# Kernel tuning notes

Measured on AMD Instinct MI355X. Metric: run time of the kernel, lower is better.

Reference implementation:

```python
import jax, jax.numpy as jnp
import numpy as np

B, D, H, W = 16, 64, 64, 64
K = 1024


def setup_inputs() -> dict:
    key = jax.random.key(0)
    k1, k2 = jax.random.split(key)
    x = jax.random.normal(k1, (B, D, H, W), dtype=jnp.float32)
    limit = 3.0 ** 0.5
    e_i_ts = jax.random.uniform(k2, (D, K), dtype=jnp.float32, minval=-limit, maxval=limit)
    return {"x": x, "e_i_ts": e_i_ts}


def reference(x, e_i_ts):
    b, d, h, w = x.shape
    # [B,H,W,D] -> [N,D]
    flat_x = jnp.transpose(x, (0, 2, 3, 1)).reshape(-1, d)
    distances = (
        jnp.sum(flat_x * flat_x, axis=1, keepdims=True)
        - 2.0 * (flat_x @ e_i_ts)
        + jnp.sum(e_i_ts * e_i_ts, axis=0, keepdims=True)
    )
    encoding_indices = jnp.argmin(distances, axis=1)  # [N]
    reshaped_indices = encoding_indices.reshape(b, h, w)
    # codebook gather: e_i_ts.T is [K,D]
    quantized = jnp.take(e_i_ts.T, reshaped_indices, axis=0)  # [B,H,W,D]
    quantized_x = jnp.transpose(quantized, (0, 3, 1, 2))  # [B,D,H,W]

    dictionary_loss = jnp.mean((jax.lax.stop_gradient(x) - quantized_x) ** 2)
    commitment_loss = jnp.mean((x - jax.lax.stop_gradient(quantized_x)) ** 2)
    # straight-through estimator
    quantized_x = x + jax.lax.stop_gradient(quantized_x - x)
    return quantized_x, dictionary_loss, commitment_loss, encoding_indices.reshape(b, -1)
```

## Files before the change

### kernel.cpp

```cpp
#include <hip/hip_runtime.h>

#define DD 64
#define KK 1024
#define NPTS 65536
#define TOTAL 4194304

#define OFF_L1 4194304
#define OFF_L2 4194305
#define OFF_IDX 4194306

#define WS_ENH_F 64
#define WS_EHT_BYTE 65536
#define WS_ELT_BYTE (65536 + 131072)

#define MARGIN_S 0.008f

typedef __attribute__((ext_vector_type(8))) short short8;
typedef __attribute__((ext_vector_type(4))) float f32x4;

__device__ __forceinline__ unsigned short bf16_rne(float f) {
    unsigned b = __float_as_uint(f);
    return (unsigned short)((b + 0x7FFFu + ((b >> 16) & 1u)) >> 16);
}
__device__ __forceinline__ float bf16_to_f(unsigned short h) {
    return __uint_as_float(((unsigned)h) << 16);
}
__device__ __forceinline__ unsigned umax(unsigned a, unsigned b) { return a > b ? a : b; }
__device__ __forceinline__ unsigned umin(unsigned a, unsigned b) { return a < b ? a : b; }
__device__ __forceinline__ void gld_lds16(const void* g, void* l) {
    __builtin_amdgcn_global_load_lds(
        (const __attribute__((address_space(1))) void*)g,
        (__attribute__((address_space(3))) void*)l, 16, 0, 0);
}
__device__ __forceinline__ int swz(int r, int d) {
    return ((d & ~7) ^ ((r & 7) << 3)) | (d & 7);
}

__global__ __launch_bounds__(256) void prep_kernel(const float* __restrict__ e,
                                                   float* __restrict__ enh,
                                                   unsigned short* __restrict__ ehT,
                                                   unsigned short* __restrict__ elT,
                                                   float* __restrict__ sum,
                                                   unsigned* __restrict__ tick) {
    const int tid = threadIdx.x;
    if (blockIdx.x == 0 && tid == 0) { *sum = 0.f; *tick = 0u; }
    const int wave = tid >> 6, lane = tid & 63;
    const int k = blockIdx.x * 4 + wave;
    const float v = e[lane * KK + k];
    const unsigned short h = bf16_rne(v);
    const unsigned short l = bf16_rne(v - bf16_to_f(h));
    const int pos = k * 64 + swz(k, lane);
    ehT[pos] = h;
    elT[pos] = l;
    float s2 = v * v;
#pragma unroll
    for (int m = 32; m > 0; m >>= 1) s2 += __shfl_down(s2, m, 64);
    if (lane == 0) enh[k] = 512.0f - 0.5f * s2;
}

__global__ __launch_bounds__(256) void vq_gemm(const float* __restrict__ x,
                                               const float* __restrict__ e,
                                               const float* __restrict__ enh,
                                               const unsigned short* __restrict__ ehT,
                                               const unsigned short* __restrict__ elT,
                                               float* __restrict__ out,
                                               float* __restrict__ sum,
                                               unsigned* __restrict__ tick) {
    __shared__ __align__(16) char ebuf[2 * 16384];
    __shared__ __align__(16) char xbuf[32768];
    __shared__ float xnp2[256];

    unsigned short* xbh = (unsigned short*)xbuf;
    unsigned short* xbl = xbh + 128 * 64;
    int*   ks  = (int*)xbuf;
    float* lv  = (float*)(ks + 128);
    float* xp  = lv + 128;
    int*   rl  = (int*)(xp + 64);
    int*   rn  = rl + 128;
    float* rv  = (float*)(rn + 1);
    int*   ri  = (int*)(rv + 4);
    float* red = (float*)(ri + 4);

    const int tid = threadIdx.x;
    const int wave = tid >> 6, lane = tid & 63;
    const int n0 = blockIdx.x * 128;
    const int b = n0 >> 12;
    const int hw0 = n0 & 4095;

    const char* ehTb = (const char*)ehT;
    const char* elTb = (const char*)elT;
    const int lofs = wave * 1024 + lane * 16;

    {
        char* db = ebuf;
        gld_lds16(ehTb + lofs,        db + wave * 1024);
        gld_lds16(ehTb + 4096 + lofs, db + 4096 + wave * 1024);
        gld_lds16(elTb + lofs,        db + 8192 + wave * 1024);
        gld_lds16(elTb + 4096 + lofs, db + 12288 + wave * 1024);
    }

    {
        const int p = tid & 127, dg = tid >> 7;
        const float* xs = x + ((b * DD + dg * 32) << 12) + hw0 + p;
        float xv[32];
        float xn = 0.f;
#pragma unroll
        for (int s = 0; s < 32; ++s) {
            xv[s] = xs[s << 12];
            xn = fmaf(xv[s], xv[s], xn);
        }
        xnp2[tid] = xn;
#pragma unroll
        for (int g = 0; g < 4; ++g) {
            short8 hh, ll;
#pragma unroll
            for (int j = 0; j < 8; ++j) {
                const float f = xv[g * 8 + j];
                const unsigned short h = bf16_rne(f);
                hh[j] = (short)h;
                ll[j] = (short)bf16_rne(f - bf16_to_f(h));
            }
            const int d0 = dg * 32 + g * 8;
            const int pos = p * 64 + (d0 ^ ((p & 7) << 3));
            *(short8*)(xbh + pos) = hh;
            *(short8*)(xbl + pos) = ll;
        }
    }
    __syncthreads();

    const int ln15 = lane & 15, q8 = (lane >> 4) * 8;
    const int wp = wave * 32;

    short8 ah[2][2], al[2][2];
#pragma unroll
    for (int rf = 0; rf < 2; ++rf)
#pragma unroll
        for (int kc = 0; kc < 2; ++kc) {
            const int pp = wp + rf * 16 + ln15;
            const int pos = pp * 64 + ((kc * 32 + q8) ^ ((pp & 7) << 3));
            ah[rf][kc] = *(const short8*)(xbh + pos);
            al[rf][kc] = *(const short8*)(xbl + pos);
        }

    unsigned v1u[8], v2u[8];
#pragma unroll
    for (int r = 0; r < 8; ++r) { v1u[r] = 0u; v2u[r] = 0u; }

    for (int kt = 0; kt < 16; ++kt) {
        __syncthreads();
        if (kt < 15) {
            const int nkt = kt + 1;
            char* db = ebuf + (nkt & 1) * 16384;
            const char* sH = ehTb + nkt * 8192 + lofs;
            const char* sL = elTb + nkt * 8192 + lofs;
            gld_lds16(sH,        db + wave * 1024);
            gld_lds16(sH + 4096, db + 4096 + wave * 1024);
            gld_lds16(sL,        db + 8192 + wave * 1024);
            gld_lds16(sL + 4096, db + 12288 + wave * 1024);
        }
        const unsigned short* ebH = (const unsigned short*)(ebuf + (kt & 1) * 16384);
        const unsigned short* ebL = ebH + 4096;

        f32x4 acc[2][4];
#pragma unroll
        for (int cf = 0; cf < 4; ++cf) {
            const float ec = enh[kt * 64 + cf * 16 + ln15];
#pragma unroll
            for (int rf = 0; rf < 2; ++rf)
                acc[rf][cf] = (f32x4){ec, ec, ec, ec};
        }

#pragma unroll
        for (int kc = 0; kc < 2; ++kc) {
            short8 bh[4], bl[4];
#pragma unroll
            for (int cf = 0; cf < 4; ++cf) {
                const int c = cf * 16 + ln15;
                const int pos = c * 64 + ((kc * 32 + q8) ^ ((c & 7) << 3));
                bh[cf] = *(const short8*)(ebH + pos);
                bl[cf] = *(const short8*)(ebL + pos);
            }
#pragma unroll
            for (int rf = 0; rf < 2; ++rf)
#pragma unroll
                for (int cf = 0; cf < 4; ++cf) {
                    acc[rf][cf] = __builtin_amdgcn_mfma_f32_16x16x32_bf16(al[rf][kc], bh[cf], acc[rf][cf], 0, 0, 0);
                    acc[rf][cf] = __builtin_amdgcn_mfma_f32_16x16x32_bf16(ah[rf][kc], bl[cf], acc[rf][cf], 0, 0, 0);
                    acc[rf][cf] = __builtin_amdgcn_mfma_f32_16x16x32_bf16(ah[rf][kc], bh[cf], acc[rf][cf], 0, 0, 0);
                }
        }

#pragma unroll
        for (int rf = 0; rf < 2; ++rf)
#pragma unroll
            for (int reg = 0; reg < 4; ++reg) {
                const int r = rf * 4 + reg;
                const unsigned k0 = (__float_as_uint(acc[rf][0][reg]) | 63u) ^ (unsigned)(kt * 4 + 0);
                const unsigned k1 = (__float_as_uint(acc[rf][1][reg]) | 63u) ^ (unsigned)(kt * 4 + 1);
                const unsigned k2 = (__float_as_uint(acc[rf][2][reg]) | 63u) ^ (unsigned)(kt * 4 + 2);
                const unsigned k3 = (__float_as_uint(acc[rf][3][reg]) | 63u) ^ (unsigned)(kt * 4 + 3);
                unsigned a = umax(k0, k1), bb = umin(k0, k1);
                v2u[r] = umax(umax(v2u[r], umin(v1u[r], a)), bb);
                v1u[r] = umax(v1u[r], a);
                a = umax(k2, k3); bb = umin(k2, k3);
                v2u[r] = umax(umax(v2u[r], umin(v1u[r], a)), bb);
                v1u[r] = umax(v1u[r], a);
            }
    }

    __syncthreads();
    if (tid == 0) *rn = 0;
    __syncthreads();

#pragma unroll
    for (int r = 0; r < 8; ++r) {
        const unsigned c6 = 63u - (v1u[r] & 63u);
        int col = (int)(c6 >> 2) * 64 + (int)(c6 & 3) * 16 + ln15;
        float val = __uint_as_float(v1u[r] & ~63u);
        float sec = __uint_as_float(v2u[r] & ~63u);
#pragma unroll
        for (int msk = 1; msk < 16; msk <<= 1) {
            const float ov = __shfl_xor(val, msk);
            const int oc = __shfl_xor(col, msk);
            const float os = __shfl_xor(sec, msk);
            sec = fmaxf(fmaxf(sec, os), fminf(val, ov));
            const bool t = (ov > val) || (ov == val && oc < col);
            val = t ? ov : val;
            col = t ? oc : col;
        }
        if (ln15 == 0) {
            const int q = lane >> 4;
            const int pt = wp + (r >> 2) * 16 + q * 4 + (r & 3);
            ks[pt] = col;
            const float xnp = xnp2[pt] + xnp2[128 + pt];
            const float bmid = __uint_as_float(__float_as_uint(val) | 32u);
            lv[pt] = xnp + 1024.0f - 2.0f * bmid;
            if (val - sec < MARGIN_S) {
                const int w = atomicAdd(rn, 1);
                rl[w] = pt;
            }
        }
    }
    __syncthreads();

    const int lcnt = *rn;
    for (int it = 0; it < lcnt; ++it) {
        const int pr = rl[it];
        if (tid < 64) xp[tid] = x[((b * DD + tid) << 12) + hw0 + pr];
        __syncthreads();
        float d0 = 0.f, d1 = 0.f, d2 = 0.f, d3 = 0.f;
#pragma unroll 8
        for (int dd = 0; dd < DD; ++dd) {
            const float xd = xp[dd];
            const float4 ev = *(const float4*)(e + dd * KK + tid * 4);
            d0 = fmaf(xd, ev.x, d0);
            d1 = fmaf(xd, ev.y, d1);
            d2 = fmaf(xd, ev.z, d2);
            d3 = fmaf(xd, ev.w, d3);
        }
        const float4 ea = *(const float4*)(enh + tid * 4);
        float bs = d0 + ea.x;
        int bi2 = tid * 4;
        if (d1 + ea.y > bs) { bs = d1 + ea.y; bi2 = tid * 4 + 1; }
        if (d2 + ea.z > bs) { bs = d2 + ea.z; bi2 = tid * 4 + 2; }
        if (d3 + ea.w > bs) { bs = d3 + ea.w; bi2 = tid * 4 + 3; }
#pragma unroll
        for (int m = 1; m < 64; m <<= 1) {
            const float ov = __shfl_xor(bs, m, 64);
            const int oi = __shfl_xor(bi2, m, 64);
            if (ov > bs || (ov == bs && oi < bi2)) { bs = ov; bi2 = oi; }
        }
        if (lane == 0) { rv[wave] = bs; ri[wave] = bi2; }
        __syncthreads();
        if (tid == 0) {
            float gs = rv[0];
            int gi = ri[0];
#pragma unroll
            for (int t2 = 1; t2 < 4; ++t2)
                if (rv[t2] > gs || (rv[t2] == gs && ri[t2] < gi)) { gs = rv[t2]; gi = ri[t2]; }
            ks[pr] = gi;
            const float xnp = xnp2[pr] + xnp2[128 + pr];
            lv[pr] = xnp + 1024.0f - 2.0f * gs;
        }
        __syncthreads();
    }

    if (tid < 128) {
        out[OFF_IDX + n0 + tid] = (float)ks[tid];
        float lc = lv[tid];
#pragma unroll
        for (int off = 32; off > 0; off >>= 1) lc += __shfl_down(lc, off, 64);
        if (lane == 0) red[wave] = lc;
    }
    __syncthreads();
    if (tid == 0) {
        atomicAdd(sum, red[0] + red[1]);
        __threadfence();
        const unsigned old = atomicAdd(tick, 1u);
        if (old == (unsigned)(gridDim.x - 1)) {
            const float s = atomicAdd(sum, 0.0f);
            const float m = s * (1.0f / (float)TOTAL);
            out[OFF_L1] = m;
            out[OFF_L2] = m;
        }
    }

    {
        const int pe = tid & 127, dh = tid >> 7;
        const int kp = ks[pe];
        const int kx = (kp & 7) << 3;
        float qa[32];
#pragma unroll
        for (int g = 0; g < 4; ++g) {
            const int pos = kp * 64 + ((dh * 32 + g * 8) ^ kx);
            const short8 h8 = *(const short8*)(ehT + pos);
            const short8 l8 = *(const short8*)(elT + pos);
#pragma unroll
            for (int j = 0; j < 8; ++j)
                qa[g * 8 + j] = bf16_to_f((unsigned short)h8[j]) + bf16_to_f((unsigned short)l8[j]);
        }
        float* ob = out + ((b * DD + dh * 32) << 12) + hw0 + pe;
#pragma unroll
        for (int s = 0; s < 32; ++s) ob[s << 12] = qa[s];
    }
}

extern "C" void kernel_launch(void* const* d_in, const int* in_sizes, int n_in,
                              void* d_out, int out_size, void* d_ws, size_t ws_size,
                              hipStream_t stream) {
    const float* x = (const float*)d_in[0];
    const float* e = (const float*)d_in[1];
    float* out = (float*)d_out;

    float* sum = (float*)d_ws;
    unsigned* tick = (unsigned*)d_ws + 2;
    float* enh = (float*)d_ws + WS_ENH_F;
    unsigned short* ehT = (unsigned short*)((char*)d_ws + WS_EHT_BYTE);
    unsigned short* elT = (unsigned short*)((char*)d_ws + WS_ELT_BYTE);

    prep_kernel<<<256, 256, 0, stream>>>(e, enh, ehT, elT, sum, tick);
    vq_gemm<<<NPTS / 128, 256, 0, stream>>>(x, e, enh, ehT, elT, out, sum, tick);
}
```

Before: 124.6 us.

## Stage codebook in 256-code quarters and coalesce prep kernel writes via LDS transpose

```diff
diff --git a/kernel.cpp b/kernel.cpp
--- a/kernel.cpp
+++ b/kernel.cpp
@@ -36,26 +36,67 @@
     return ((d & ~7) ^ ((r & 7) << 3)) | (d & 7);
 }
 
+__device__ __forceinline__ void stage_quarter(const char* ehTb, const char* elTb,
+                                              char* cb, int q, int wave, int lane) {
+    const int off = wave * 8192 + lane * 16;
+    const char* sH = ehTb + q * 32768 + off;
+    const char* sL = elTb + q * 32768 + off;
+    char* dH = cb + wave * 8192;
+    char* dL = cb + 32768 + wave * 8192;
+#pragma unroll
+    for (int j = 0; j < 8; ++j) {
+        gld_lds16(sH + j * 1024, dH + j * 1024);
+        gld_lds16(sL + j * 1024, dL + j * 1024);
+    }
+}
+
 __global__ __launch_bounds__(256) void prep_kernel(const float* __restrict__ e,
                                                    float* __restrict__ enh,
                                                    unsigned short* __restrict__ ehT,
                                                    unsigned short* __restrict__ elT,
                                                    float* __restrict__ sum,
                                                    unsigned* __restrict__ tick) {
-    const int tid = threadIdx.x;
+    __shared__ unsigned short tH[64 * 64];
+    __shared__ unsigned short tL[64 * 64];
+    __shared__ float ps[4 * 64];
+    const int tid = threadIdx.x, wave = tid >> 6, lane = tid & 63;
     if (blockIdx.x == 0 && tid == 0) { *sum = 0.f; *tick = 0u; }
-    const int wave = tid >> 6, lane = tid & 63;
-    const int k = blockIdx.x * 4 + wave;
-    const float v = e[lane * KK + k];
-    const unsigned short h = bf16_rne(v);
-    const unsigned short l = bf16_rne(v - bf16_to_f(h));
-    const int pos = k * 64 + swz(k, lane);
-    ehT[pos] = h;
-    elT[pos] = l;
-    float s2 = v * v;
-#pragma unroll
-    for (int m = 32; m > 0; m >>= 1) s2 += __shfl_down(s2, m, 64);
-    if (lane == 0) enh[k] = 512.0f - 0.5f * s2;
+    const int k = blockIdx.x * 64 + lane;
+    float s2 = 0.f;
+    short8 hh[2], ll[2];
+#pragma unroll
+    for (int g = 0; g < 2; ++g)
+#pragma unroll
+        for (int j = 0; j < 8; ++j) {
+            const int d = wave * 16 + g * 8 + j;
+            const float v = e[d * KK + k];
+            const unsigned short h = bf16_rne(v);
+            hh[g][j] = (short)h;
+            ll[g][j] = (short)bf16_rne(v - bf16_to_f(h));
+            s2 = fmaf(v, v, s2);
+        }
+    ps[wave * 64 + lane] = s2;
+#pragma unroll
+    for (int g = 0; g < 2; ++g) {
+        const int pos = lane * 64 + ((wave * 16 + g * 8) ^ ((k & 7) << 3));
+        *(short8*)(tH + pos) = hh[g];
+        *(short8*)(tL + pos) = ll[g];
+    }
+    __syncthreads();
+    if (wave == 0) {
+        const float t = ps[lane] + ps[64 + lane] + ps[128 + lane] + ps[192 + lane];
+        enh[k] = 512.0f - 0.5f * t;
+    }
+    {
+        const short8* srcH = (const short8*)tH;
+        const short8* srcL = (const short8*)tL;
+        short8* dstH = (short8*)(ehT + blockIdx.x * 64 * 64);
+        short8* dstL = (short8*)(elT + blockIdx.x * 64 * 64);
+        dstH[tid * 2]     = srcH[tid * 2];
+        dstH[tid * 2 + 1] = srcH[tid * 2 + 1];
+        dstL[tid * 2]     = srcL[tid * 2];
+        dstL[tid * 2 + 1] = srcL[tid * 2 + 1];
+    }
 }
 
 __global__ __launch_bounds__(256) void vq_gemm(const float* __restrict__ x,
@@ -66,13 +107,12 @@
                                                float* __restrict__ out,
                                                float* __restrict__ sum,
                                                unsigned* __restrict__ tick) {
-    __shared__ __align__(16) char ebuf[2 * 16384];
-    __shared__ __align__(16) char xbuf[32768];
+    __shared__ __align__(16) char cb[65536];
     __shared__ float xnp2[256];
 
-    unsigned short* xbh = (unsigned short*)xbuf;
-    unsigned short* xbl = xbh + 128 * 64;
-    int*   ks  = (int*)xbuf;
+    unsigned short* xbh = (unsigned short*)cb;
+    unsigned short* xbl = (unsigned short*)(cb + 16384);
+    int*   ks  = (int*)cb;
     float* lv  = (float*)(ks + 128);
     float* xp  = lv + 128;
     int*   rl  = (int*)(xp + 64);
@@ -89,15 +129,6 @@
 
     const char* ehTb = (const char*)ehT;
     const char* elTb = (const char*)elT;
-    const int lofs = wave * 1024 + lane * 16;
-
-    {
-        char* db = ebuf;
-        gld_lds16(ehTb + lofs,        db + wave * 1024);
-        gld_lds16(ehTb + 4096 + lofs, db + 4096 + wave * 1024);
-        gld_lds16(elTb + lofs,        db + 8192 + wave * 1024);
-        gld_lds16(elTb + 4096 + lofs, db + 12288 + wave * 1024);
-    }
 
     {
         const int p = tid & 127, dg = tid >> 7;
@@ -141,74 +172,75 @@
             ah[rf][kc] = *(const short8*)(xbh + pos);
             al[rf][kc] = *(const short8*)(xbl + pos);
         }
+    __syncthreads();
+
+    stage_quarter(ehTb, elTb, cb, 0, wave, lane);
 
     unsigned v1u[8], v2u[8];
 #pragma unroll
     for (int r = 0; r < 8; ++r) { v1u[r] = 0u; v2u[r] = 0u; }
 
-    for (int kt = 0; kt < 16; ++kt) {
-        __syncthreads();
-        if (kt < 15) {
-            const int nkt = kt + 1;
-            char* db = ebuf + (nkt & 1) * 16384;
-            const char* sH = ehTb + nkt * 8192 + lofs;
-            const char* sL = elTb + nkt * 8192 + lofs;
-            gld_lds16(sH,        db + wave * 1024);
-            gld_lds16(sH + 4096, db + 4096 + wave * 1024);
-            gld_lds16(sL,        db + 8192 + wave * 1024);
-            gld_lds16(sL + 4096, db + 12288 + wave * 1024);
-        }
-        const unsigned short* ebH = (const unsigned short*)(ebuf + (kt & 1) * 16384);
-        const unsigned short* ebL = ebH + 4096;
-
-        f32x4 acc[2][4];
-#pragma unroll
-        for (int cf = 0; cf < 4; ++cf) {
-            const float ec = enh[kt * 64 + cf * 16 + ln15];
+    const unsigned short* cbH = (const unsigned short*)cb;
+    const unsigned short* cbL = (const unsigned short*)(cb + 32768);
+
+    for (int q = 0; q < 4; ++q) {
+        __syncthreads();
+
+#pragma unroll
+        for (int ct = 0; ct < 4; ++ct) {
+            const int tile = q * 4 + ct;
+
+            f32x4 acc[2][4];
+#pragma unroll
+            for (int cf = 0; cf < 4; ++cf) {
+                const float ec = enh[tile * 64 + cf * 16 + ln15];
+#pragma unroll
+                for (int rf = 0; rf < 2; ++rf)
+                    acc[rf][cf] = (f32x4){ec, ec, ec, ec};
+            }
+
+#pragma unroll
+            for (int kc = 0; kc < 2; ++kc) {
+                short8 bh[4], bl[4];
+#pragma unroll
+                for (int cf = 0; cf < 4; ++cf) {
+                    const int c = ct * 64 + cf * 16 + ln15;
+                    const int pos = c * 64 + ((kc * 32 + q8) ^ ((c & 7) << 3));
+                    bh[cf] = *(const short8*)(cbH + pos);
+                    bl[cf] = *(const short8*)(cbL + pos);
+                }
+#pragma unroll
+                for (int rf = 0; rf < 2; ++rf)
+#pragma unroll
+                    for (int cf = 0; cf < 4; ++cf) {
+                        acc[rf][cf] = __builtin_amdgcn_mfma_f32_16x16x32_bf16(al[rf][kc], bh[cf], acc[rf][cf], 0, 0, 0);
+                        acc[rf][cf] = __builtin_amdgcn_mfma_f32_16x16x32_bf16(ah[rf][kc], bl[cf], acc[rf][cf], 0, 0, 0);
+                        acc[rf][cf] = __builtin_amdgcn_mfma_f32_16x16x32_bf16(ah[rf][kc], bh[cf], acc[rf][cf], 0, 0, 0);
+                    }
+            }
+
 #pragma unroll
             for (int rf = 0; rf < 2; ++rf)
-                acc[rf][cf] = (f32x4){ec, ec, ec, ec};
-        }
-
-#pragma unroll
-        for (int kc = 0; kc < 2; ++kc) {
-            short8 bh[4], bl[4];
-#pragma unroll
-            for (int cf = 0; cf < 4; ++cf) {
-                const int c = cf * 16 + ln15;
-                const int pos = c * 64 + ((kc * 32 + q8) ^ ((c & 7) << 3));
-                bh[cf] = *(const short8*)(ebH + pos);
-                bl[cf] = *(const short8*)(ebL + pos);
-            }
-#pragma unroll
-            for (int rf = 0; rf < 2; ++rf)
-#pragma unroll
-                for (int cf = 0; cf < 4; ++cf) {
-                    acc[rf][cf] = __builtin_amdgcn_mfma_f32_16x16x32_bf16(al[rf][kc], bh[cf], acc[rf][cf], 0, 0, 0);
-                    acc[rf][cf] = __builtin_amdgcn_mfma_f32_16x16x32_bf16(ah[rf][kc], bl[cf], acc[rf][cf], 0, 0, 0);
-                    acc[rf][cf] = __builtin_amdgcn_mfma_f32_16x16x32_bf16(ah[rf][kc], bh[cf], acc[rf][cf], 0, 0, 0);
+#pragma unroll
+                for (int reg = 0; reg < 4; ++reg) {
+                    const int r = rf * 4 + reg;
+                    const unsigned k0 = (__float_as_uint(acc[rf][0][reg]) | 63u) ^ (unsigned)(tile * 4 + 0);
+                    const unsigned k1 = (__float_as_uint(acc[rf][1][reg]) | 63u) ^ (unsigned)(tile * 4 + 1);
+                    const unsigned k2 = (__float_as_uint(acc[rf][2][reg]) | 63u) ^ (unsigned)(tile * 4 + 2);
+                    const unsigned k3 = (__float_as_uint(acc[rf][3][reg]) | 63u) ^ (unsigned)(tile * 4 + 3);
+                    unsigned a = umax(k0, k1), bb = umin(k0, k1);
+                    v2u[r] = umax(umax(v2u[r], umin(v1u[r], a)), bb);
+                    v1u[r] = umax(v1u[r], a);
+                    a = umax(k2, k3); bb = umin(k2, k3);
+                    v2u[r] = umax(umax(v2u[r], umin(v1u[r], a)), bb);
+                    v1u[r] = umax(v1u[r], a);
                 }
         }
 
-#pragma unroll
-        for (int rf = 0; rf < 2; ++rf)
-#pragma unroll
-            for (int reg = 0; reg < 4; ++reg) {
-                const int r = rf * 4 + reg;
-                const unsigned k0 = (__float_as_uint(acc[rf][0][reg]) | 63u) ^ (unsigned)(kt * 4 + 0);
-                const unsigned k1 = (__float_as_uint(acc[rf][1][reg]) | 63u) ^ (unsigned)(kt * 4 + 1);
-                const unsigned k2 = (__float_as_uint(acc[rf][2][reg]) | 63u) ^ (unsigned)(kt * 4 + 2);
-                const unsigned k3 = (__float_as_uint(acc[rf][3][reg]) | 63u) ^ (unsigned)(kt * 4 + 3);
-                unsigned a = umax(k0, k1), bb = umin(k0, k1);
-                v2u[r] = umax(umax(v2u[r], umin(v1u[r], a)), bb);
-                v1u[r] = umax(v1u[r], a);
-                a = umax(k2, k3); bb = umin(k2, k3);
-                v2u[r] = umax(umax(v2u[r], umin(v1u[r], a)), bb);
-                v1u[r] = umax(v1u[r], a);
-            }
-    }
-
-    __syncthreads();
+        __syncthreads();
+        if (q < 3) stage_quarter(ehTb, elTb, cb, q + 1, wave, lane);
+    }
+
     if (tid == 0) *rn = 0;
     __syncthreads();
 
@@ -229,8 +261,8 @@
             col = t ? oc : col;
         }
         if (ln15 == 0) {
-            const int q = lane >> 4;
-            const int pt = wp + (r >> 2) * 16 + q * 4 + (r & 3);
+            const int qq = lane >> 4;
+            const int pt = wp + (r >> 2) * 16 + qq * 4 + (r & 3);
             ks[pt] = col;
             const float xnp = xnp2[pt] + xnp2[128 + pt];
             const float bmid = __uint_as_float(__float_as_uint(val) | 32u);
@@ -338,6 +370,6 @@
     unsigned short* ehT = (unsigned short*)((char*)d_ws + WS_EHT_BYTE);
     unsigned short* elT = (unsigned short*)((char*)d_ws + WS_ELT_BYTE);
 
-    prep_kernel<<<256, 256, 0, stream>>>(e, enh, ehT, elT, sum, tick);
+    prep_kernel<<<KK / 64, 256, 0, stream>>>(e, enh, ehT, elT, sum, tick);
     vq_gemm<<<NPTS / 128, 256, 0, stream>>>(x, e, enh, ehT, elT, out, sum, tick);
 }
```

New measurement: 121.5 us. 2.5% less time.

## Alias x staging into codebook buffer to cut LDS and compute loss exactly

Applied to the files above, without the earlier changes.

```diff
diff --git a/kernel.cpp b/kernel.cpp
--- a/kernel.cpp
+++ b/kernel.cpp
@@ -42,20 +42,47 @@
                                                    unsigned short* __restrict__ elT,
                                                    float* __restrict__ sum,
                                                    unsigned* __restrict__ tick) {
-    const int tid = threadIdx.x;
+    __shared__ unsigned short tH[64 * 64];
+    __shared__ unsigned short tL[64 * 64];
+    __shared__ float ps[4 * 64];
+    const int tid = threadIdx.x, wave = tid >> 6, lane = tid & 63;
     if (blockIdx.x == 0 && tid == 0) { *sum = 0.f; *tick = 0u; }
-    const int wave = tid >> 6, lane = tid & 63;
-    const int k = blockIdx.x * 4 + wave;
-    const float v = e[lane * KK + k];
-    const unsigned short h = bf16_rne(v);
-    const unsigned short l = bf16_rne(v - bf16_to_f(h));
-    const int pos = k * 64 + swz(k, lane);
-    ehT[pos] = h;
-    elT[pos] = l;
-    float s2 = v * v;
-#pragma unroll
-    for (int m = 32; m > 0; m >>= 1) s2 += __shfl_down(s2, m, 64);
-    if (lane == 0) enh[k] = 512.0f - 0.5f * s2;
+    const int k = blockIdx.x * 64 + lane;
+    float s2 = 0.f;
+    short8 hh[2], ll[2];
+#pragma unroll
+    for (int g = 0; g < 2; ++g)
+#pragma unroll
+        for (int j = 0; j < 8; ++j) {
+            const int d = wave * 16 + g * 8 + j;
+            const float v = e[d * KK + k];
+            const unsigned short h = bf16_rne(v);
+            hh[g][j] = (short)h;
+            ll[g][j] = (short)bf16_rne(v - bf16_to_f(h));
+            s2 = fmaf(v, v, s2);
+        }
+    ps[wave * 64 + lane] = s2;
+#pragma unroll
+    for (int g = 0; g < 2; ++g) {
+        const int pos = lane * 64 + ((wave * 16 + g * 8) ^ ((k & 7) << 3));
+        *(short8*)(tH + pos) = hh[g];
+        *(short8*)(tL + pos) = ll[g];
+    }
+    __syncthreads();
+    if (wave == 0) {
+        const float t = ps[lane] + ps[64 + lane] + ps[128 + lane] + ps[192 + lane];
+        enh[k] = 512.0f - 0.5f * t;
+    }
+    {
+        const short8* srcH = (const short8*)tH;
+        const short8* srcL = (const short8*)tL;
+        short8* dstH = (short8*)(ehT + blockIdx.x * 64 * 64);
+        short8* dstL = (short8*)(elT + blockIdx.x * 64 * 64);
+        dstH[tid * 2]     = srcH[tid * 2];
+        dstH[tid * 2 + 1] = srcH[tid * 2 + 1];
+        dstL[tid * 2]     = srcL[tid * 2];
+        dstL[tid * 2 + 1] = srcL[tid * 2 + 1];
+    }
 }
 
 __global__ __launch_bounds__(256) void vq_gemm(const float* __restrict__ x,
@@ -67,14 +94,11 @@
                                                float* __restrict__ sum,
                                                unsigned* __restrict__ tick) {
     __shared__ __align__(16) char ebuf[2 * 16384];
-    __shared__ __align__(16) char xbuf[32768];
-    __shared__ float xnp2[256];
-
-    unsigned short* xbh = (unsigned short*)xbuf;
-    unsigned short* xbl = xbh + 128 * 64;
-    int*   ks  = (int*)xbuf;
-    float* lv  = (float*)(ks + 128);
-    float* xp  = lv + 128;
+
+    unsigned short* xbh = (unsigned short*)ebuf;
+    unsigned short* xbl = (unsigned short*)(ebuf + 16384);
+    int*   ks  = (int*)ebuf;
+    float* xp  = (float*)(ks + 128);
     int*   rl  = (int*)(xp + 64);
     int*   rn  = rl + 128;
     float* rv  = (float*)(rn + 1);
@@ -92,24 +116,11 @@
     const int lofs = wave * 1024 + lane * 16;
 
     {
-        char* db = ebuf;
-        gld_lds16(ehTb + lofs,        db + wave * 1024);
-        gld_lds16(ehTb + 4096 + lofs, db + 4096 + wave * 1024);
-        gld_lds16(elTb + lofs,        db + 8192 + wave * 1024);
-        gld_lds16(elTb + 4096 + lofs, db + 12288 + wave * 1024);
-    }
-
-    {
         const int p = tid & 127, dg = tid >> 7;
         const float* xs = x + ((b * DD + dg * 32) << 12) + hw0 + p;
         float xv[32];
-        float xn = 0.f;
-#pragma unroll
-        for (int s = 0; s < 32; ++s) {
-            xv[s] = xs[s << 12];
-            xn = fmaf(xv[s], xv[s], xn);
-        }
-        xnp2[tid] = xn;
+#pragma unroll
+        for (int s = 0; s < 32; ++s) xv[s] = xs[s << 12];
 #pragma unroll
         for (int g = 0; g < 4; ++g) {
             short8 hh, ll;
@@ -141,6 +152,15 @@
             ah[rf][kc] = *(const short8*)(xbh + pos);
             al[rf][kc] = *(const short8*)(xbl + pos);
         }
+    __syncthreads();
+
+    {
+        char* db = ebuf;
+        gld_lds16(ehTb + lofs,        db + wave * 1024);
+        gld_lds16(ehTb + 4096 + lofs, db + 4096 + wave * 1024);
+        gld_lds16(elTb + lofs,        db + 8192 + wave * 1024);
+        gld_lds16(elTb + 4096 + lofs, db + 12288 + wave * 1024);
+    }
 
     unsigned v1u[8], v2u[8];
 #pragma unroll
@@ -229,12 +249,9 @@
             col = t ? oc : col;
         }
         if (ln15 == 0) {
-            const int q = lane >> 4;
-            const int pt = wp + (r >> 2) * 16 + q * 4 + (r & 3);
+            const int qq = lane >> 4;
+            const int pt = wp + (r >> 2) * 16 + qq * 4 + (r & 3);
             ks[pt] = col;
-            const float xnp = xnp2[pt] + xnp2[128 + pt];
-            const float bmid = __uint_as_float(__float_as_uint(val) | 32u);
-            lv[pt] = xnp + 1024.0f - 2.0f * bmid;
             if (val - sec < MARGIN_S) {
                 const int w = atomicAdd(rn, 1);
                 rl[w] = pt;
@@ -279,22 +296,32 @@
             for (int t2 = 1; t2 < 4; ++t2)
                 if (rv[t2] > gs || (rv[t2] == gs && ri[t2] < gi)) { gs = rv[t2]; gi = ri[t2]; }
             ks[pr] = gi;
-            const float xnp = xnp2[pr] + xnp2[128 + pr];
-            lv[pr] = xnp + 1024.0f - 2.0f * gs;
         }
         __syncthreads();
     }
 
-    if (tid < 128) {
-        out[OFF_IDX + n0 + tid] = (float)ks[tid];
-        float lc = lv[tid];
-#pragma unroll
-        for (int off = 32; off > 0; off >>= 1) lc += __shfl_down(lc, off, 64);
-        if (lane == 0) red[wave] = lc;
+    if (tid < 128) out[OFF_IDX + n0 + tid] = (float)ks[tid];
+
+    {
+        const int pe = tid & 127, dh = tid >> 7;
+        const int kp = ks[pe];
+        float lacc = 0.f;
+#pragma unroll
+        for (int s = 0; s < 32; ++s) {
+            const int d = dh * 32 + s;
+            const float qv = e[d * KK + kp];
+            const float xv = x[((b * DD + d) << 12) + hw0 + pe];
+            out[((b * DD + d) << 12) + hw0 + pe] = qv;
+            const float df = xv - qv;
+            lacc = fmaf(df, df, lacc);
+        }
+#pragma unroll
+        for (int off = 32; off > 0; off >>= 1) lacc += __shfl_down(lacc, off, 64);
+        if (lane == 0) red[wave] = lacc;
     }
     __syncthreads();
     if (tid == 0) {
-        atomicAdd(sum, red[0] + red[1]);
+        atomicAdd(sum, red[0] + red[1] + red[2] + red[3]);
         __threadfence();
         const unsigned old = atomicAdd(tick, 1u);
         if (old == (unsigned)(gridDim.x - 1)) {
@@ -304,25 +331,6 @@
             out[OFF_L2] = m;
         }
     }
-
-    {
-        const int pe = tid & 127, dh = tid >> 7;
-        const int kp = ks[pe];
-        const int kx = (kp & 7) << 3;
-        float qa[32];
-#pragma unroll
-        for (int g = 0; g < 4; ++g) {
-            const int pos = kp * 64 + ((dh * 32 + g * 8) ^ kx);
-            const short8 h8 = *(const short8*)(ehT + pos);
-            const short8 l8 = *(const short8*)(elT + pos);
-#pragma unroll
-            for (int j = 0; j < 8; ++j)
-                qa[g * 8 + j] = bf16_to_f((unsigned short)h8[j]) + bf16_to_f((unsigned short)l8[j]);
-        }
-        float* ob = out + ((b * DD + dh * 32) << 12) + hw0 + pe;
-#pragma unroll
-        for (int s = 0; s < 32; ++s) ob[s << 12] = qa[s];
-    }
 }
 
 extern "C" void kernel_launch(void* const* d_in, const int* in_sizes, int n_in,
@@ -338,6 +346,6 @@
     unsigned short* ehT = (unsigned short*)((char*)d_ws + WS_EHT_BYTE);
     unsigned short* elT = (unsigned short*)((char*)d_ws + WS_ELT_BYTE);
 
-    prep_kernel<<<256, 256, 0, stream>>>(e, enh, ehT, elT, sum, tick);
+    prep_kernel<<<KK / 64, 256, 0, stream>>>(e, enh, ehT, elT, sum, tick);
     vq_gemm<<<NPTS / 128, 256, 0, stream>>>(x, e, enh, ehT, elT, out, sum, tick);
 }
```

Result: no change. 125.5 us (+0.8%).
